# Kernel tuning notes

Hardware: AMD Instinct MI355X
Metric: run time of the kernel (lower is better)

The kernel has to match this reference:

```python
import jax, jax.numpy as jnp
import numpy as np

B, T = 2, 1000
IN_DIM, OUT_DIM = 257, 514
D_MODEL, D_STATE, D_CONV, EXPAND = 512, 16, 4, 2
D_INNER = EXPAND * D_MODEL          # 1024
DT_RANK = (D_MODEL + 15) // 16      # ceil(512/16) = 32
N_LAYER = 4
K_DC = 31                            # depthwise conv kernel in MambaDCLayer


def layer_norm(x, g, b, eps=1e-5):
    mu = jnp.mean(x, axis=-1, keepdims=True)
    var = jnp.mean((x - mu) ** 2, axis=-1, keepdims=True)
    return (x - mu) * jax.lax.rsqrt(var + eps) * g + b


def dw_conv1d(x, w, b, pad):
    # x: (B, T, C), w: (C, K) depthwise, pad: (left, right)
    y = jax.lax.conv_general_dilated(
        x.transpose(0, 2, 1), w[:, None, :], (1,), [pad],
        dimension_numbers=('NCH', 'OIH', 'NCH'), feature_group_count=w.shape[0])
    return (y + b[None, :, None]).transpose(0, 2, 1)


def mamba_block(x, W_in, conv_w, conv_b, W_x, W_dt, b_dt, A_log, Dp, W_out):
    # x: (B, T, d_model)
    xz = x @ W_in                               # (B, T, 2*D_INNER)
    xin, z = jnp.split(xz, 2, axis=-1)
    xin = dw_conv1d(xin, conv_w, conv_b, (D_CONV - 1, 0))  # causal depthwise conv
    xin = jax.nn.silu(xin)                      # (B, T, D_INNER)
    proj = xin @ W_x                            # (B, T, DT_RANK + 2*D_STATE)
    dt = jax.nn.softplus(proj[..., :DT_RANK] @ W_dt + b_dt)  # (B, T, D_INNER)
    Bm = proj[..., DT_RANK:DT_RANK + D_STATE]   # (B, T, D_STATE)
    Cm = proj[..., DT_RANK + D_STATE:]          # (B, T, D_STATE)
    A = -jnp.exp(A_log)                         # (D_INNER, D_STATE)
    dA = jnp.exp(dt[..., None] * A)             # (B, T, D_INNER, D_STATE)
    dBu = (dt * xin)[..., None] * Bm[:, :, None, :]  # (B, T, D_INNER, D_STATE)

    def step(h, inp):
        dA_t, dBu_t, C_t = inp
        h = dA_t * h + dBu_t
        return h, jnp.einsum('bds,bs->bd', h, C_t)

    h0 = jnp.zeros((x.shape[0], D_INNER, D_STATE), x.dtype)
    _, ys = jax.lax.scan(step, h0, (dA.transpose(1, 0, 2, 3),
                                    dBu.transpose(1, 0, 2, 3),
                                    Cm.transpose(1, 0, 2)))
    y = ys.transpose(1, 0, 2) + xin * Dp        # (B, T, D_INNER)
    y = y * jax.nn.silu(z)
    return y @ W_out                            # (B, T, d_model)


def setup_inputs() -> dict:
    key = jax.random.key(0)
    ks = iter(jax.random.split(key, 32))
    n = lambda shape, s=0.02: jax.random.normal(next(ks), shape, jnp.float32) * s
    return {
        'x': jax.random.normal(next(ks), (B, T, IN_DIM), jnp.float32),
        'lengths': jnp.full((B,), T, jnp.int32),
        'w_in0': n((IN_DIM, D_MODEL)),
        'ln_in_g': jnp.ones((D_MODEL,), jnp.float32),
        'ln_in_b': jnp.zeros((D_MODEL,), jnp.float32),
        'ln1_g': jnp.ones((N_LAYER, D_MODEL), jnp.float32),
        'ln1_b': jnp.zeros((N_LAYER, D_MODEL), jnp.float32),
        'W_inproj': n((N_LAYER, D_MODEL, 2 * D_INNER)),
        'conv_w': n((N_LAYER, D_INNER, D_CONV), 0.1),
        'conv_b': jnp.zeros((N_LAYER, D_INNER), jnp.float32),
        'W_xproj': n((N_LAYER, D_INNER, DT_RANK + 2 * D_STATE)),
        'W_dt': n((N_LAYER, DT_RANK, D_INNER), 0.1),
        'b_dt': jnp.full((N_LAYER, D_INNER), -4.6, jnp.float32),
        'A_log': jnp.tile(jnp.log(jnp.arange(1, D_STATE + 1, dtype=jnp.float32)),
                          (N_LAYER, D_INNER, 1)),
        'D': jnp.ones((N_LAYER, D_INNER), jnp.float32),
        'W_mo': n((N_LAYER, D_INNER, D_MODEL)),
        'ln2_g': jnp.ones((N_LAYER, D_MODEL), jnp.float32),
        'ln2_b': jnp.zeros((N_LAYER, D_MODEL), jnp.float32),
        'dc_w': n((N_LAYER, D_MODEL, K_DC), 0.1),
        'dc_b': jnp.zeros((N_LAYER, D_MODEL), jnp.float32),
        'w_out': n((D_MODEL, OUT_DIM)),
        'b_out': jnp.zeros((OUT_DIM,), jnp.float32),
    }


def reference(x, lengths, w_in0, ln_in_g, ln_in_b, ln1_g, ln1_b, W_inproj,
              conv_w, conv_b, W_xproj, W_dt, b_dt, A_log, D, W_mo,
              ln2_g, ln2_b, dc_w, dc_b, w_out, b_out):
    seq_mask = jnp.arange(x.shape[1]) < lengths[:, None]  # (B, T) bool
    h = jax.nn.relu(layer_norm(x @ w_in0, ln_in_g, ln_in_b))
    for i in range(N_LAYER):
        a = h + mamba_block(layer_norm(h, ln1_g[i], ln1_b[i]),
                            W_inproj[i], conv_w[i], conv_b[i], W_xproj[i],
                            W_dt[i], b_dt[i], A_log[i], D[i], W_mo[i])
        c = dw_conv1d(layer_norm(a, ln2_g[i], ln2_b[i]), dc_w[i], dc_b[i],
                      (K_DC // 2, K_DC // 2))  # 'same' padding
        h = a + c
    out = h @ w_out + b_out  # MagcIRM -> linear output head
    # lengths == T so output[seq_mask] is a full flatten to (B*T, OUT_DIM)
    out_flat = out.reshape(-1, out.shape[-1])
    return out_flat, seq_mask
```

## Files before the change

### kernel.cpp

```cpp
#include <hip/hip_runtime.h>
#include <cstdint>
#include <cstddef>

#define DEVI static __device__ __forceinline__

typedef unsigned short ushort_t;
typedef __attribute__((ext_vector_type(8))) short short8;
typedef __attribute__((ext_vector_type(4))) float f32x4;

DEVI float sp_softplus(float x) { return x > 20.f ? x : log1pf(__expf(x)); }
DEVI float silu_f(float x)      { return x / (1.f + __expf(-x)); }

DEVI ushort_t f2b(float v) {
    uint32_t u = __builtin_bit_cast(uint32_t, v);
    u += 0x7FFFu + ((u >> 16) & 1u);
    return (ushort_t)(u >> 16);
}
DEVI float b2f(ushort_t u) {
    uint32_t x = ((uint32_t)u) << 16;
    return __builtin_bit_cast(float, x);
}

DEVI void gload16(const ushort_t* g, ushort_t* l) {
    __builtin_amdgcn_global_load_lds(
        (const __attribute__((address_space(1))) unsigned int*)g,
        (__attribute__((address_space(3))) unsigned int*)l, 16, 0, 0);
}

#define NC 40
#define CL 25

template<bool RELU, bool OUTB16>
__global__ __launch_bounds__(256) void ln_k(const float* __restrict__ x,
                                            const float* __restrict__ g,
                                            const float* __restrict__ b,
                                            void* __restrict__ yv, int M)
{
    int wid  = threadIdx.x >> 6;
    int lane = threadIdx.x & 63;
    int row  = blockIdx.x * 4 + wid;
    if (row >= M) return;
    const float* xr = x + (size_t)row * 512;
    float4 v0 = *(const float4*)(xr + lane * 8);
    float4 v1 = *(const float4*)(xr + lane * 8 + 4);
    float vals[8] = {v0.x, v0.y, v0.z, v0.w, v1.x, v1.y, v1.z, v1.w};
    float s = 0.f;
#pragma unroll
    for (int i = 0; i < 8; i++) s += vals[i];
#pragma unroll
    for (int off = 1; off < 64; off <<= 1) s += __shfl_xor(s, off);
    float mu = s * (1.f / 512.f);
    float q = 0.f;
#pragma unroll
    for (int i = 0; i < 8; i++) { float d = vals[i] - mu; q += d * d; }
#pragma unroll
    for (int off = 1; off < 64; off <<= 1) q += __shfl_xor(q, off);
    float rstd = rsqrtf(q * (1.f / 512.f) + 1e-5f);
#pragma unroll
    for (int i = 0; i < 8; i++) {
        int c = lane * 8 + i;
        float o = (vals[i] - mu) * rstd * g[c] + b[c];
        if (RELU) o = fmaxf(o, 0.f);
        if (OUTB16) ((ushort_t*)yv)[(size_t)row * 512 + c] = f2b(o);
        else        ((float*)yv)[(size_t)row * 512 + c] = o;
    }
}

__global__ __launch_bounds__(256) void cvt_x_k(const float* __restrict__ x,
                                               ushort_t* __restrict__ xb)
{
    int e = blockIdx.x * 256 + threadIdx.x;
    if (e >= 2000 * 320) return;
    int k = e % 320, row = e / 320;
    xb[e] = (k < 257) ? f2b(x[(size_t)row * 257 + k]) : (ushort_t)0;
}

__global__ __launch_bounds__(256) void prep_small_k(const float* __restrict__ conv_w,
                                                    const float* __restrict__ dc_w,
                                                    const float* __restrict__ W_xproj,
                                                    float* __restrict__ cwt,
                                                    float* __restrict__ dcwt,
                                                    ushort_t* __restrict__ wxb)
{
    int e = blockIdx.x * 256 + threadIdx.x;
    if (e < 16384) {
        int l = e >> 12, rem = e & 4095, k = rem >> 10, d = rem & 1023;
        cwt[e] = conv_w[l * 4096 + d * 4 + k];
        return;
    }
    e -= 16384;
    if (e < 63488) {
        int l = e / 15872, rem = e % 15872, k = rem / 512, m = rem % 512;
        dcwt[e] = dc_w[l * 15872 + m * 31 + k];
        return;
    }
    e -= 63488;
    if (e < 262144) wxb[e] = f2b(W_xproj[e]);
}

__global__ __launch_bounds__(256) void tr_w_k(const float* __restrict__ src,
                                              ushort_t* __restrict__ dst,
                                              int Ktrue, int N, int ldo, int srcld,
                                              size_t sstride, size_t dstride)
{
    __shared__ float tile[32][33];
    src += blockIdx.z * sstride;
    dst += blockIdx.z * dstride;
    int n0 = blockIdx.x * 32, k0 = blockIdx.y * 32;
    int tx = threadIdx.x & 31, ty = threadIdx.x >> 5;
#pragma unroll
    for (int r = 0; r < 4; r++) {
        int k = k0 + ty + r * 8, n = n0 + tx;
        tile[ty + r * 8][tx] = (k < Ktrue && n < N) ? src[(size_t)k * srcld + n] : 0.f;
    }
    __syncthreads();
#pragma unroll
    for (int r = 0; r < 4; r++) {
        int n = n0 + ty + r * 8;
        if (n < N) dst[(size_t)n * ldo + k0 + tx] = f2b(tile[tx][ty + r * 8]);
    }
}

template<bool BIAS, int ACT, bool RES, bool OUTF32, bool OUTB16>
__global__ __launch_bounds__(256) void gemm6(
    const ushort_t* __restrict__ A, int lda,
    const ushort_t* __restrict__ Bt, int ldb,
    const float* __restrict__ bias,
    const float* __restrict__ R, int ldr,
    float* __restrict__ C, int ldc,
    ushort_t* __restrict__ C2, int ldc2,
    int M, int N, int K,
    size_t aStr, size_t bStr, size_t cStr)
{
    __shared__ ushort_t As[3][64 * 64];
    __shared__ ushort_t Bs[3][64 * 64];
    A  += blockIdx.z * aStr;
    Bt += blockIdx.z * bStr;
    C  += blockIdx.z * cStr;
    C2 += blockIdx.z * cStr;

    int tid = threadIdx.x;
    int wid = tid >> 6, l = tid & 63;
    int wr = wid >> 1, wc = wid & 1;
    int lk = l >> 4, lr = l & 15;
    int rhalf = tid >> 3, oct = tid & 7;

    int nwg = gridDim.x * gridDim.y;
    int bid = blockIdx.y * gridDim.x + blockIdx.x;
    {
        int q = nwg >> 3, r = nwg & 7;
        int xcd = bid & 7, lo = bid >> 3;
        bid = (xcd < r ? xcd * (q + 1) : r * (q + 1) + (xcd - r) * q) + lo;
    }
    int bx = bid % gridDim.x, by = bid / gridDim.x;
    int bm = by * 64, bn = bx * 64;

    f32x4 acc[2][2];
#pragma unroll
    for (int m = 0; m < 2; m++)
#pragma unroll
        for (int n = 0; n < 2; n++) acc[m][n] = (f32x4){0.f, 0.f, 0.f, 0.f};

    auto stage = [&](int buf, int k0) {
#pragma unroll
        for (int p = 0; p < 2; p++) {
            int row = p * 32 + rhalf;
            int cg = oct ^ (row & 7);
            gload16(A + (size_t)(bm + row) * lda + k0 + cg * 8,
                    &As[buf][p * 2048 + tid * 8]);
        }
#pragma unroll
        for (int p = 0; p < 2; p++) {
            int row = p * 32 + rhalf;
            int cg = oct ^ (row & 7);
            gload16(Bt + (size_t)(bn + row) * ldb + k0 + cg * 8,
                    &Bs[buf][p * 2048 + tid * 8]);
        }
    };

    auto compute = [&](int buf) {
#pragma unroll
        for (int kk = 0; kk < 2; kk++) {
            short8 af[2], bf[2];
#pragma unroll
            for (int m = 0; m < 2; m++) {
                int row = wr * 32 + m * 16 + lr;
                int sl = (kk * 4 + lk) ^ (row & 7);
                af[m] = *(const short8*)&As[buf][row * 64 + sl * 8];
            }
#pragma unroll
            for (int n = 0; n < 2; n++) {
                int col = wc * 32 + n * 16 + lr;
                int sl = (kk * 4 + lk) ^ (col & 7);
                bf[n] = *(const short8*)&Bs[buf][col * 64 + sl * 8];
            }
#pragma unroll
            for (int m = 0; m < 2; m++)
#pragma unroll
                for (int n = 0; n < 2; n++)
                    acc[m][n] = __builtin_amdgcn_mfma_f32_16x16x32_bf16(
                        af[m], bf[n], acc[m][n], 0, 0, 0);
        }
    };

    int nt = K >> 6;
    stage(0, 0);
    if (nt > 1) stage(1, 64);
    for (int t = 0; t < nt; t++) {
        if (t + 1 < nt) asm volatile("s_waitcnt vmcnt(4)" ::: "memory");
        else            asm volatile("s_waitcnt vmcnt(0)" ::: "memory");
        __builtin_amdgcn_s_barrier();
        if (t + 2 < nt) stage((t + 2) % 3, (t + 2) * 64);
        compute(t % 3);
    }

#pragma unroll
    for (int m = 0; m < 2; m++) {
#pragma unroll
        for (int n = 0; n < 2; n++) {
            int gn = bn + wc * 32 + n * 16 + lr;
            if (gn >= N) continue;
#pragma unroll
            for (int r = 0; r < 4; r++) {
                int gm = bm + wr * 32 + m * 16 + lk * 4 + r;
                if (gm >= M) continue;
                float v = acc[m][n][r];
                if (ACT == 2) {
                    if (gn < 1024) C2[(size_t)gm * ldc2 + gn] = f2b(sp_softplus(v + bias[gn]));
                    else ((float*)R)[(size_t)gm * ldr + (gn - 1024) + 32] = v;
                    continue;
                }
                if (BIAS) v += bias[gn];
                if (ACT == 1) v = sp_softplus(v);
                if (RES) v += R[(size_t)gm * ldr + gn];
                if (OUTF32) C[(size_t)gm * ldc + gn] = v;
                if (OUTB16) C2[(size_t)gm * ldc2 + gn] = f2b(v);
            }
        }
    }
}

__global__ __launch_bounds__(256) void conv4_silu_k(const ushort_t* __restrict__ xzb,
                                                    const float* __restrict__ cwt,
                                                    const float* __restrict__ bias,
                                                    ushort_t* __restrict__ xinb)
{
    int e = blockIdx.x * 256 + threadIdx.x;
    if (e >= 2000 * 128) return;
    int dg = (e & 127) * 8;
    int row = e >> 7;
    int b = row >= 1000 ? 1 : 0;
    int t = row - b * 1000;
    float acc[8];
#pragma unroll
    for (int j = 0; j < 8; j++) acc[j] = bias[dg + j];
#pragma unroll
    for (int k = 0; k < 4; k++) {
        int tt = t - 3 + k;
        if (tt < 0) continue;
        short8 v = *(const short8*)&xzb[(size_t)(b * 1000 + tt) * 2048 + dg];
#pragma unroll
        for (int j = 0; j < 8; j++)
            acc[j] += b2f((ushort_t)v[j]) * cwt[k * 1024 + dg + j];
    }
    short8 o;
#pragma unroll
    for (int j = 0; j < 8; j++) o[j] = (short)f2b(silu_f(acc[j]));
    *(short8*)&xinb[(size_t)row * 1024 + dg] = o;
}

__global__ __launch_bounds__(256) void scan_part1(const ushort_t* __restrict__ dt,
                                                  const ushort_t* __restrict__ xin,
                                                  const float* __restrict__ proj,
                                                  const float* __restrict__ A_log,
                                                  float* __restrict__ hloc,
                                                  float* __restrict__ sc)
{
    __shared__ ushort_t s_dt[CL][64], s_x[CL][64];
    __shared__ float s_B[CL][16];
    int d0 = blockIdx.x * 64;
    int c  = blockIdx.y;
    int b  = blockIdx.z;
    int tid = threadIdx.x;
    int ch = tid >> 2, st4 = tid & 3;
    int d = d0 + ch;
    int base = b * 1000 + c * CL;
    for (int lin = tid; lin < CL * 8; lin += 256) {
        int r = lin >> 3, q = lin & 7;
        size_t row = (size_t)(base + r);
        *(short8*)&s_dt[r][q * 8] = *(const short8*)&dt[row * 1024 + d0 + q * 8];
        *(short8*)&s_x[r][q * 8]  = *(const short8*)&xin[row * 1024 + d0 + q * 8];
    }
    for (int lin = tid; lin < CL * 16; lin += 256) {
        int r = lin >> 4, j = lin & 15;
        s_B[r][j] = proj[(size_t)(base + r) * 64 + 32 + j];
    }
    float4 alog = *(const float4*)&A_log[d * 16 + st4 * 4];
    float a_s[4] = {-__expf(alog.x), -__expf(alog.y), -__expf(alog.z), -__expf(alog.w)};
    __syncthreads();
    float h[4] = {0.f, 0.f, 0.f, 0.f};
    float sdt = 0.f;
#pragma unroll 5
    for (int t = 0; t < CL; t++) {
        float dtv = b2f(s_dt[t][ch]);
        float xv  = b2f(s_x[t][ch]);
        float4 Bv = *(const float4*)&s_B[t][st4 * 4];
        float dx = dtv * xv;
        sdt += dtv;
        h[0] = __expf(dtv * a_s[0]) * h[0] + dx * Bv.x;
        h[1] = __expf(dtv * a_s[1]) * h[1] + dx * Bv.y;
        h[2] = __expf(dtv * a_s[2]) * h[2] + dx * Bv.z;
        h[3] = __expf(dtv * a_s[3]) * h[3] + dx * Bv.w;
    }
    *(float4*)&hloc[((size_t)(b * NC + c) << 14) + ((size_t)d << 4) + st4 * 4] =
        (float4){h[0], h[1], h[2], h[3]};
    if (st4 == 0) sc[(b * NC + c) * 1024 + d] = sdt;
}

__global__ __launch_bounds__(256) void scan_combine(const float* __restrict__ A_log,
                                                    float* __restrict__ hloc,
                                                    const float* __restrict__ sc)
{
    int e = blockIdx.x * 256 + threadIdx.x;
    if (e >= 2 * 16384) return;
    int b = e >> 14;
    int rem = e & 16383;
    int dd = rem >> 4;
    float a_s = -__expf(A_log[rem]);
    float H = hloc[((size_t)(b * NC) << 14) + rem];
    for (int c = 1; c < NC; c++) {
        size_t idx = ((size_t)(b * NC + c) << 14) + rem;
        H = hloc[idx] + __expf(a_s * sc[(b * NC + c) * 1024 + dd]) * H;
        hloc[idx] = H;
    }
}

__global__ __launch_bounds__(256) void scan_part2(const ushort_t* __restrict__ dt,
                                                  const ushort_t* __restrict__ xin,
                                                  const float* __restrict__ proj,
                                                  const float* __restrict__ A_log,
                                                  const float* __restrict__ hend,
                                                  const float* __restrict__ Dp,
                                                  const ushort_t* __restrict__ xzb,
                                                  ushort_t* __restrict__ ysb)
{
    __shared__ ushort_t s_dt[CL][64], s_x[CL][64], s_y[CL][64];
    __shared__ float s_B[CL][16], s_C[CL][16];
    __shared__ float s_Dp[64];
    int d0 = blockIdx.x * 64;
    int c  = blockIdx.y;
    int b  = blockIdx.z;
    int tid = threadIdx.x;
    int ch = tid >> 2, st4 = tid & 3;
    int d = d0 + ch;
    int base = b * 1000 + c * CL;
    if (tid < 64) s_Dp[tid] = Dp[d0 + tid];
    for (int lin = tid; lin < CL * 8; lin += 256) {
        int r = lin >> 3, q = lin & 7;
        size_t row = (size_t)(base + r);
        *(short8*)&s_dt[r][q * 8] = *(const short8*)&dt[row * 1024 + d0 + q * 8];
        *(short8*)&s_x[r][q * 8]  = *(const short8*)&xin[row * 1024 + d0 + q * 8];
    }
    for (int lin = tid; lin < CL * 16; lin += 256) {
        int r = lin >> 4, j = lin & 15;
        s_B[r][j] = proj[(size_t)(base + r) * 64 + 32 + j];
        s_C[r][j] = proj[(size_t)(base + r) * 64 + 48 + j];
    }
    float4 alog = *(const float4*)&A_log[d * 16 + st4 * 4];
    float a_s[4] = {-__expf(alog.x), -__expf(alog.y), -__expf(alog.z), -__expf(alog.w)};
    float h[4] = {0.f, 0.f, 0.f, 0.f};
    if (c > 0) {
        float4 hv = *(const float4*)&hend[((size_t)(b * NC + c - 1) << 14)
                                          + ((size_t)d << 4) + st4 * 4];
        h[0] = hv.x; h[1] = hv.y; h[2] = hv.z; h[3] = hv.w;
    }
    __syncthreads();
#pragma unroll 5
    for (int t = 0; t < CL; t++) {
        float dtv = b2f(s_dt[t][ch]);
        float xv  = b2f(s_x[t][ch]);
        float4 Bv = *(const float4*)&s_B[t][st4 * 4];
        float4 Cv = *(const float4*)&s_C[t][st4 * 4];
        float dx = dtv * xv;
        h[0] = __expf(dtv * a_s[0]) * h[0] + dx * Bv.x;
        h[1] = __expf(dtv * a_s[1]) * h[1] + dx * Bv.y;
        h[2] = __expf(dtv * a_s[2]) * h[2] + dx * Bv.z;
        h[3] = __expf(dtv * a_s[3]) * h[3] + dx * Bv.w;
        float p = h[0] * Cv.x + h[1] * Cv.y + h[2] * Cv.z + h[3] * Cv.w;
        p += __shfl_xor(p, 1);
        p += __shfl_xor(p, 2);
        if (st4 == 0) s_y[t][ch] = f2b(p);
    }
    __syncthreads();
    for (int lin = tid; lin < CL * 8; lin += 256) {
        int r = lin >> 3, q = lin & 7;
        size_t row = (size_t)(base + r);
        int dd = d0 + q * 8;
        short8 yv = *(const short8*)&s_y[r][q * 8];
        short8 xv = *(const short8*)&s_x[r][q * 8];
        short8 zv = *(const short8*)&xzb[row * 2048 + 1024 + dd];
        short8 ov;
#pragma unroll
        for (int j = 0; j < 8; j++) {
            float o = (b2f((ushort_t)yv[j]) + b2f((ushort_t)xv[j]) * s_Dp[q * 8 + j])
                      * silu_f(b2f((ushort_t)zv[j]));
            ov[j] = (short)f2b(o);
        }
        *(short8*)&ysb[row * 1024 + dd] = ov;
    }
}

__global__ __launch_bounds__(256) void dcconv31_k(const float* __restrict__ ln,
                                                  const float* __restrict__ a,
                                                  const float* __restrict__ dcwt,
                                                  const float* __restrict__ bias,
                                                  float* __restrict__ h,
                                                  ushort_t* __restrict__ hb)
{
    int e = blockIdx.x * 256 + threadIdx.x;
    if (e >= 2000 * 512) return;
    int m = e & 511;
    int row = e >> 9;
    int b = row >= 1000 ? 1 : 0;
    int t = row - b * 1000;
    float acc = bias[m];
#pragma unroll
    for (int k = 0; k < 31; k++) {
        int tt = t - 15 + k;
        if (tt >= 0 && tt < 1000)
            acc += ln[((size_t)(b * 1000 + tt)) * 512 + m] * dcwt[k * 512 + m];
    }
    float v = a[e] + acc;
    h[e] = v;
    hb[e] = f2b(v);
}

__global__ void mask_k(const int* __restrict__ lengths, float* __restrict__ out)
{
    int i = blockIdx.x * 256 + threadIdx.x;
    if (i >= 2000) return;
    out[i] = ((i % 1000) < lengths[i / 1000]) ? 1.f : 0.f;
}

extern "C" void kernel_launch(void* const* d_in, const int* in_sizes, int n_in,
                              void* d_out, int out_size, void* d_ws, size_t ws_size,
                              hipStream_t stream)
{
    const float* x       = (const float*)d_in[0];
    const int*   lengths = (const int*)  d_in[1];
    const float* w_in0   = (const float*)d_in[2];
    const float* ln_in_g = (const float*)d_in[3];
    const float* ln_in_b = (const float*)d_in[4];
    const float* ln1_g   = (const float*)d_in[5];
    const float* ln1_b   = (const float*)d_in[6];
    const float* W_inproj= (const float*)d_in[7];
    const float* conv_w  = (const float*)d_in[8];
    const float* conv_b  = (const float*)d_in[9];
    const float* W_xproj = (const float*)d_in[10];
    const float* W_dt    = (const float*)d_in[11];
    const float* b_dt    = (const float*)d_in[12];
    const float* A_log   = (const float*)d_in[13];
    const float* Dp      = (const float*)d_in[14];
    const float* W_mo    = (const float*)d_in[15];
    const float* ln2_g   = (const float*)d_in[16];
    const float* ln2_b   = (const float*)d_in[17];
    const float* dc_w    = (const float*)d_in[18];
    const float* dc_b    = (const float*)d_in[19];
    const float* w_out   = (const float*)d_in[20];
    const float* b_out   = (const float*)d_in[21];

    char* p = (char*)d_ws;
    auto alloc_f = [&](size_t n) { float* r = (float*)p; p += n * 4; return r; };
    auto alloc_b = [&](size_t n) { ushort_t* r = (ushort_t*)p; p += n * 2; return r; };

    float* h    = alloc_f(2048 * 512);
    float* lnb  = alloc_f(2048 * 512);
    float* proj = alloc_f(2048 * 64);
    float* av   = alloc_f(2048 * 512);
    float* hloc = alloc_f((size_t)2 * NC * 16384);
    float* sc   = alloc_f((size_t)2 * NC * 1024);
    float* cwt  = alloc_f(4 * 4 * 1024);
    float* dcwt = alloc_f(4 * 31 * 512);
    ushort_t* xbf   = alloc_b(2048 * 320);
    ushort_t* lnbb  = alloc_b(2048 * 512);
    ushort_t* xzb   = alloc_b(2048 * 2048);
    ushort_t* xinb  = alloc_b(2048 * 1024);
    ushort_t* dtbb  = alloc_b(2048 * 1024);
    ushort_t* ysb   = alloc_b(2048 * 1024);
    ushort_t* hb    = alloc_b(2048 * 512);
    ushort_t* wt_in0 = alloc_b(512 * 320);
    ushort_t* wt_in  = alloc_b((size_t)4 * 2048 * 512);
    ushort_t* wt_dt  = alloc_b((size_t)4 * 1024 * 64);
    ushort_t* wt_mo  = alloc_b((size_t)4 * 512 * 1024);
    ushort_t* wt_out = alloc_b(576 * 512);
    ushort_t* wxb    = alloc_b((size_t)4 * 1024 * 64);
    ushort_t* wt_big = alloc_b((size_t)4 * 1152 * 1024);

    dim3 blk(256);

    cvt_x_k<<<(2000 * 320 + 255) / 256, blk, 0, stream>>>(x, xbf);
    prep_small_k<<<(16384 + 63488 + 262144 + 255) / 256, blk, 0, stream>>>(
        conv_w, dc_w, W_xproj, cwt, dcwt, wxb);
    tr_w_k<<<dim3(16, 10, 1), blk, 0, stream>>>(w_in0, wt_in0, 257, 512, 320, 512, 0, 0);
    tr_w_k<<<dim3(64, 16, 4), blk, 0, stream>>>(W_inproj, wt_in, 512, 2048, 512, 2048,
                                                (size_t)512 * 2048, (size_t)2048 * 512);
    tr_w_k<<<dim3(32, 2, 4),  blk, 0, stream>>>(W_dt, wt_dt, 32, 1024, 64, 1024,
                                                (size_t)32 * 1024, (size_t)1024 * 64);
    tr_w_k<<<dim3(16, 32, 4), blk, 0, stream>>>(W_mo, wt_mo, 1024, 512, 1024, 512,
                                                (size_t)1024 * 512, (size_t)512 * 1024);
    tr_w_k<<<dim3(17, 16, 1), blk, 0, stream>>>(w_out, wt_out, 512, 514, 512, 514, 0, 0);
    tr_w_k<<<dim3(1, 32, 4),  blk, 0, stream>>>(W_xproj + 32, wt_big + (size_t)1024 * 1024,
                                                1024, 32, 1024, 64,
                                                (size_t)1024 * 64, (size_t)1152 * 1024);
    gemm6<false, 0, false, false, true><<<dim3(16, 16, 4), blk, 0, stream>>>(
        wt_dt, 64, wxb, 64, nullptr, nullptr, 0, nullptr, 0, wt_big, 1024,
        1024, 1024, 64,
        (size_t)1024 * 64, (size_t)1024 * 64, (size_t)1152 * 1024);

    gemm6<false, 0, false, true, false><<<dim3(8, 32), blk, 0, stream>>>(
        xbf, 320, wt_in0, 320, nullptr, nullptr, 0, lnb, 512, nullptr, 0,
        2000, 512, 320, 0, 0, 0);
    ln_k<true, false><<<500, blk, 0, stream>>>(lnb, ln_in_g, ln_in_b, h, 2000);

    for (int i = 0; i < 4; i++) {
        const float* Al = A_log + (size_t)i * 16384;
        ln_k<false, true><<<500, blk, 0, stream>>>(h, ln1_g + i * 512, ln1_b + i * 512,
                                                   lnbb, 2000);
        gemm6<false, 0, false, false, true><<<dim3(32, 32), blk, 0, stream>>>(
            lnbb, 512, wt_in + (size_t)i * 2048 * 512, 512,
            nullptr, nullptr, 0, nullptr, 0, xzb, 2048, 2000, 2048, 512, 0, 0, 0);
        conv4_silu_k<<<1000, blk, 0, stream>>>(xzb, cwt + i * 4096,
                                               conv_b + i * 1024, xinb);
        gemm6<false, 2, false, false, false><<<dim3(17, 32), blk, 0, stream>>>(
            xinb, 1024, wt_big + (size_t)i * 1152 * 1024, 1024,
            b_dt + i * 1024, proj, 64, nullptr, 0, dtbb, 1024, 2000, 1056, 1024, 0, 0, 0);
        scan_part1<<<dim3(16, NC, 2), blk, 0, stream>>>(dtbb, xinb, proj, Al, hloc, sc);
        scan_combine<<<128, blk, 0, stream>>>(Al, hloc, sc);
        scan_part2<<<dim3(16, NC, 2), blk, 0, stream>>>(dtbb, xinb, proj, Al, hloc,
                                                        Dp + i * 1024, xzb, ysb);
        gemm6<false, 0, true, true, false><<<dim3(8, 32), blk, 0, stream>>>(
            ysb, 1024, wt_mo + (size_t)i * 512 * 1024, 1024,
            nullptr, h, 512, av, 512, nullptr, 0, 2000, 512, 1024, 0, 0, 0);
        ln_k<false, false><<<500, blk, 0, stream>>>(av, ln2_g + i * 512, ln2_b + i * 512,
                                                    lnb, 2000);
        dcconv31_k<<<4000, blk, 0, stream>>>(lnb, av, dcwt + i * 31 * 512,
                                             dc_b + i * 512, h, hb);
    }

    gemm6<true, 0, false, true, false><<<dim3(9, 32), blk, 0, stream>>>(
        hb, 512, wt_out, 512, b_out, nullptr, 0, (float*)d_out, 514, nullptr, 0,
        2000, 514, 512, 0, 0, 0);
    mask_k<<<8, blk, 0, stream>>>(lengths, (float*)d_out + 2000 * 514);
}
```

Measured before the change: 516.7 us.

## Fuse chunked scan passes into one kernel with inter-block flag sync; bf16 LN2 output

Merges the three-kernel chunked selective scan (local pass, serial combine, second pass) into one kernel. Chunk-0 blocks spin until all chunks publish local states, then propagate the carried state and raise per-chunk flags that later-chunk blocks wait on. This removes two launches and reloading dt/x/B into shared memory, but depends on all blocks being co-resident to avoid deadlock, and the combine serialises through chunk-0 blocks with a syncthreads per chunk. Separately, the second layernorm now writes bf16 and the depthwise conv reads bf16, halving that traffic at some precision cost.

```diff
diff --git a/kernel.cpp b/kernel.cpp
--- a/kernel.cpp
+++ b/kernel.cpp
@@ -269,22 +269,27 @@
     *(short8*)&xinb[(size_t)row * 1024 + dg] = o;
 }
 
-__global__ __launch_bounds__(256) void scan_part1(const ushort_t* __restrict__ dt,
-                                                  const ushort_t* __restrict__ xin,
-                                                  const float* __restrict__ proj,
-                                                  const float* __restrict__ A_log,
-                                                  float* __restrict__ hloc,
-                                                  float* __restrict__ sc)
-{
-    __shared__ ushort_t s_dt[CL][64], s_x[CL][64];
-    __shared__ float s_B[CL][16];
-    int d0 = blockIdx.x * 64;
-    int c  = blockIdx.y;
-    int b  = blockIdx.z;
+__global__ __launch_bounds__(256, 5) void scan_fused(
+    const ushort_t* __restrict__ dt, const ushort_t* __restrict__ xin,
+    const float* __restrict__ proj, const float* __restrict__ A_log,
+    const float* __restrict__ Dp, const ushort_t* __restrict__ xzb,
+    ushort_t* __restrict__ ysb, float* __restrict__ hloc,
+    float* __restrict__ sc, unsigned* __restrict__ cnt,
+    unsigned* __restrict__ pflag)
+{
+    __shared__ ushort_t s_dt[CL][64], s_x[CL][64], s_y[CL][64];
+    __shared__ float s_B[CL][16], s_C[CL][16];
+    __shared__ float s_Dp[64];
+    int x = blockIdx.x, c = blockIdx.y, b = blockIdx.z;
+    int d0 = x * 64;
     int tid = threadIdx.x;
     int ch = tid >> 2, st4 = tid & 3;
     int d = d0 + ch;
     int base = b * 1000 + c * CL;
+    unsigned* mycnt = cnt + b * 16 + x;
+    unsigned* mypf  = pflag + (size_t)(b * 16 + x) * NC;
+
+    if (tid < 64) s_Dp[tid] = Dp[d0 + tid];
     for (int lin = tid; lin < CL * 8; lin += 256) {
         int r = lin >> 3, q = lin & 7;
         size_t row = (size_t)(base + r);
@@ -294,10 +299,12 @@
     for (int lin = tid; lin < CL * 16; lin += 256) {
         int r = lin >> 4, j = lin & 15;
         s_B[r][j] = proj[(size_t)(base + r) * 64 + 32 + j];
+        s_C[r][j] = proj[(size_t)(base + r) * 64 + 48 + j];
     }
     float4 alog = *(const float4*)&A_log[d * 16 + st4 * 4];
     float a_s[4] = {-__expf(alog.x), -__expf(alog.y), -__expf(alog.z), -__expf(alog.w)};
     __syncthreads();
+
     float h[4] = {0.f, 0.f, 0.f, 0.f};
     float sdt = 0.f;
 #pragma unroll 5
@@ -312,69 +319,56 @@
         h[2] = __expf(dtv * a_s[2]) * h[2] + dx * Bv.z;
         h[3] = __expf(dtv * a_s[3]) * h[3] + dx * Bv.w;
     }
-    *(float4*)&hloc[((size_t)(b * NC + c) << 14) + ((size_t)d << 4) + st4 * 4] =
-        (float4){h[0], h[1], h[2], h[3]};
+    size_t hidx = ((size_t)(b * NC + c) << 14) + ((size_t)d << 4) + st4 * 4;
+    *(float4*)&hloc[hidx] = (float4){h[0], h[1], h[2], h[3]};
     if (st4 == 0) sc[(b * NC + c) * 1024 + d] = sdt;
-}
-
-__global__ __launch_bounds__(256) void scan_combine(const float* __restrict__ A_log,
-                                                    float* __restrict__ hloc,
-                                                    const float* __restrict__ sc)
-{
-    int e = blockIdx.x * 256 + threadIdx.x;
-    if (e >= 2 * 16384) return;
-    int b = e >> 14;
-    int rem = e & 16383;
-    int dd = rem >> 4;
-    float a_s = -__expf(A_log[rem]);
-    float H = hloc[((size_t)(b * NC) << 14) + rem];
-    for (int c = 1; c < NC; c++) {
-        size_t idx = ((size_t)(b * NC + c) << 14) + rem;
-        H = hloc[idx] + __expf(a_s * sc[(b * NC + c) * 1024 + dd]) * H;
-        hloc[idx] = H;
-    }
-}
-
-__global__ __launch_bounds__(256) void scan_part2(const ushort_t* __restrict__ dt,
-                                                  const ushort_t* __restrict__ xin,
-                                                  const float* __restrict__ proj,
-                                                  const float* __restrict__ A_log,
-                                                  const float* __restrict__ hend,
-                                                  const float* __restrict__ Dp,
-                                                  const ushort_t* __restrict__ xzb,
-                                                  ushort_t* __restrict__ ysb)
-{
-    __shared__ ushort_t s_dt[CL][64], s_x[CL][64], s_y[CL][64];
-    __shared__ float s_B[CL][16], s_C[CL][16];
-    __shared__ float s_Dp[64];
-    int d0 = blockIdx.x * 64;
-    int c  = blockIdx.y;
-    int b  = blockIdx.z;
-    int tid = threadIdx.x;
-    int ch = tid >> 2, st4 = tid & 3;
-    int d = d0 + ch;
-    int base = b * 1000 + c * CL;
-    if (tid < 64) s_Dp[tid] = Dp[d0 + tid];
-    for (int lin = tid; lin < CL * 8; lin += 256) {
-        int r = lin >> 3, q = lin & 7;
-        size_t row = (size_t)(base + r);
-        *(short8*)&s_dt[r][q * 8] = *(const short8*)&dt[row * 1024 + d0 + q * 8];
-        *(short8*)&s_x[r][q * 8]  = *(const short8*)&xin[row * 1024 + d0 + q * 8];
-    }
-    for (int lin = tid; lin < CL * 16; lin += 256) {
-        int r = lin >> 4, j = lin & 15;
-        s_B[r][j] = proj[(size_t)(base + r) * 64 + 32 + j];
-        s_C[r][j] = proj[(size_t)(base + r) * 64 + 48 + j];
-    }
-    float4 alog = *(const float4*)&A_log[d * 16 + st4 * 4];
-    float a_s[4] = {-__expf(alog.x), -__expf(alog.y), -__expf(alog.z), -__expf(alog.w)};
-    float h[4] = {0.f, 0.f, 0.f, 0.f};
-    if (c > 0) {
-        float4 hv = *(const float4*)&hend[((size_t)(b * NC + c - 1) << 14)
+    __threadfence();
+    __syncthreads();
+    if (tid == 0) {
+        atomicAdd(mycnt, 1u);
+        if (c == 0) atomicExch(&mypf[0], 1u);
+    }
+
+    float hs[4] = {0.f, 0.f, 0.f, 0.f};
+    if (c == 0) {
+        while (atomicAdd(mycnt, 0u) < NC) __builtin_amdgcn_s_sleep(2);
+        __threadfence();
+        float H[4] = {h[0], h[1], h[2], h[3]};
+        for (int cb = 1; cb < NC; cb += 8) {
+            float4 hv[8]; float sv[8];
+#pragma unroll
+            for (int j = 0; j < 8; j++) {
+                if (cb + j < NC) {
+                    hv[j] = *(const float4*)&hloc[((size_t)(b * NC + cb + j) << 14)
+                                                  + ((size_t)d << 4) + st4 * 4];
+                    sv[j] = sc[(b * NC + cb + j) * 1024 + d];
+                }
+            }
+#pragma unroll
+            for (int j = 0; j < 8; j++) {
+                if (cb + j < NC) {
+                    H[0] = hv[j].x + __expf(a_s[0] * sv[j]) * H[0];
+                    H[1] = hv[j].y + __expf(a_s[1] * sv[j]) * H[1];
+                    H[2] = hv[j].z + __expf(a_s[2] * sv[j]) * H[2];
+                    H[3] = hv[j].w + __expf(a_s[3] * sv[j]) * H[3];
+                    *(float4*)&hloc[((size_t)(b * NC + cb + j) << 14)
+                                    + ((size_t)d << 4) + st4 * 4] =
+                        (float4){H[0], H[1], H[2], H[3]};
+                    __threadfence();
+                    __syncthreads();
+                    if (tid == 0) atomicExch(&mypf[cb + j], 1u);
+                }
+            }
+        }
+    } else {
+        while (atomicAdd(&mypf[c - 1], 0u) == 0u) __builtin_amdgcn_s_sleep(2);
+        __threadfence();
+        float4 hv = *(const float4*)&hloc[((size_t)(b * NC + c - 1) << 14)
                                           + ((size_t)d << 4) + st4 * 4];
-        h[0] = hv.x; h[1] = hv.y; h[2] = hv.z; h[3] = hv.w;
-    }
-    __syncthreads();
+        hs[0] = hv.x; hs[1] = hv.y; hs[2] = hv.z; hs[3] = hv.w;
+    }
+
+    h[0] = hs[0]; h[1] = hs[1]; h[2] = hs[2]; h[3] = hs[3];
 #pragma unroll 5
     for (int t = 0; t < CL; t++) {
         float dtv = b2f(s_dt[t][ch]);
@@ -410,7 +404,7 @@
     }
 }
 
-__global__ __launch_bounds__(256) void dcconv31_k(const float* __restrict__ ln,
+__global__ __launch_bounds__(256) void dcconv31_k(const ushort_t* __restrict__ ln,
                                                   const float* __restrict__ a,
                                                   const float* __restrict__ dcwt,
                                                   const float* __restrict__ bias,
@@ -428,7 +422,7 @@
     for (int k = 0; k < 31; k++) {
         int tt = t - 15 + k;
         if (tt >= 0 && tt < 1000)
-            acc += ln[((size_t)(b * 1000 + tt)) * 512 + m] * dcwt[k * 512 + m];
+            acc += b2f(ln[((size_t)(b * 1000 + tt)) * 512 + m]) * dcwt[k * 512 + m];
     }
     float v = a[e] + acc;
     h[e] = v;
@@ -472,6 +466,7 @@
     char* p = (char*)d_ws;
     auto alloc_f = [&](size_t n) { float* r = (float*)p; p += n * 4; return r; };
     auto alloc_b = [&](size_t n) { ushort_t* r = (ushort_t*)p; p += n * 2; return r; };
+    auto alloc_u = [&](size_t n) { unsigned* r = (unsigned*)p; p += n * 4; return r; };
 
     float* h    = alloc_f(2048 * 512);
     float* lnb  = alloc_f(2048 * 512);
@@ -481,6 +476,7 @@
     float* sc   = alloc_f((size_t)2 * NC * 1024);
     float* cwt  = alloc_f(4 * 4 * 1024);
     float* dcwt = alloc_f(4 * 31 * 512);
+    unsigned* flags = alloc_u(4 * (32 + 32 * NC));
     ushort_t* xbf   = alloc_b(2048 * 320);
     ushort_t* lnbb  = alloc_b(2048 * 512);
     ushort_t* xzb   = alloc_b(2048 * 2048);
@@ -497,6 +493,8 @@
     ushort_t* wt_big = alloc_b((size_t)4 * 1152 * 1024);
 
     dim3 blk(256);
+
+    hipMemsetAsync(flags, 0, (size_t)4 * (32 + 32 * NC) * 4, stream);
 
     cvt_x_k<<<(2000 * 320 + 255) / 256, blk, 0, stream>>>(x, xbf);
     prep_small_k<<<(16384 + 63488 + 262144 + 255) / 256, blk, 0, stream>>>(
@@ -524,6 +522,8 @@
 
     for (int i = 0; i < 4; i++) {
         const float* Al = A_log + (size_t)i * 16384;
+        unsigned* cnt_i = flags + (size_t)i * (32 + 32 * NC);
+        unsigned* pf_i  = cnt_i + 32;
         ln_k<false, true><<<500, blk, 0, stream>>>(h, ln1_g + i * 512, ln1_b + i * 512,
                                                    lnbb, 2000);
         gemm6<false, 0, false, false, true><<<dim3(32, 32), blk, 0, stream>>>(
@@ -534,16 +534,14 @@
         gemm6<false, 2, false, false, false><<<dim3(17, 32), blk, 0, stream>>>(
             xinb, 1024, wt_big + (size_t)i * 1152 * 1024, 1024,
             b_dt + i * 1024, proj, 64, nullptr, 0, dtbb, 1024, 2000, 1056, 1024, 0, 0, 0);
-        scan_part1<<<dim3(16, NC, 2), blk, 0, stream>>>(dtbb, xinb, proj, Al, hloc, sc);
-        scan_combine<<<128, blk, 0, stream>>>(Al, hloc, sc);
-        scan_part2<<<dim3(16, NC, 2), blk, 0, stream>>>(dtbb, xinb, proj, Al, hloc,
-                                                        Dp + i * 1024, xzb, ysb);
+        scan_fused<<<dim3(16, NC, 2), blk, 0, stream>>>(
+            dtbb, xinb, proj, Al, Dp + i * 1024, xzb, ysb, hloc, sc, cnt_i, pf_i);
         gemm6<false, 0, true, true, false><<<dim3(8, 32), blk, 0, stream>>>(
             ysb, 1024, wt_mo + (size_t)i * 512 * 1024, 1024,
             nullptr, h, 512, av, 512, nullptr, 0, 2000, 512, 1024, 0, 0, 0);
-        ln_k<false, false><<<500, blk, 0, stream>>>(av, ln2_g + i * 512, ln2_b + i * 512,
-                                                    lnb, 2000);
-        dcconv31_k<<<4000, blk, 0, stream>>>(lnb, av, dcwt + i * 31 * 512,
+        ln_k<false, true><<<500, blk, 0, stream>>>(av, ln2_g + i * 512, ln2_b + i * 512,
+                                                   lnbb, 2000);
+        dcconv31_k<<<4000, blk, 0, stream>>>(lnbb, av, dcwt + i * 31 * 512,
                                              dc_b + i * 512, h, hb);
     }
 
```

Result: slower. 1.783 ms (+245.0%).

## Unfold precomposed W_x·W_dt into two-stage x_proj then dt_proj GEMMs

Applied to the files above, without the earlier changes.

Drops the setup-time precomposition of W_xproj and W_dt into a 1152-wide weight. Instead each layer runs a small 64-column x_proj GEMM, which writes proj in fp32 plus a bf16 copy of the dt-rank slice, then a K=64 dt GEMM with bias and softplus. This cuts the FLOPs of the per-layer wide GEMM and removes the setup GEMM, at the cost of an extra launch and a very low-parallelism 64-column GEMM. Separately, the second LayerNorm now writes bf16 and the 31-tap conv reads bf16, halving that traffic at some precision cost.

```diff
diff --git a/kernel.cpp b/kernel.cpp
--- a/kernel.cpp
+++ b/kernel.cpp
@@ -77,10 +77,8 @@
 
 __global__ __launch_bounds__(256) void prep_small_k(const float* __restrict__ conv_w,
                                                     const float* __restrict__ dc_w,
-                                                    const float* __restrict__ W_xproj,
                                                     float* __restrict__ cwt,
-                                                    float* __restrict__ dcwt,
-                                                    ushort_t* __restrict__ wxb)
+                                                    float* __restrict__ dcwt)
 {
     int e = blockIdx.x * 256 + threadIdx.x;
     if (e < 16384) {
@@ -92,10 +90,7 @@
     if (e < 63488) {
         int l = e / 15872, rem = e % 15872, k = rem / 512, m = rem % 512;
         dcwt[e] = dc_w[l * 15872 + m * 31 + k];
-        return;
-    }
-    e -= 63488;
-    if (e < 262144) wxb[e] = f2b(W_xproj[e]);
+    }
 }
 
 __global__ __launch_bounds__(256) void tr_w_k(const float* __restrict__ src,
@@ -225,9 +220,10 @@
                 int gm = bm + wr * 32 + m * 16 + lk * 4 + r;
                 if (gm >= M) continue;
                 float v = acc[m][n][r];
-                if (ACT == 2) {
-                    if (gn < 1024) C2[(size_t)gm * ldc2 + gn] = f2b(sp_softplus(v + bias[gn]));
-                    else ((float*)R)[(size_t)gm * ldr + (gn - 1024) + 32] = v;
+                if (ACT == 3) {
+                    if (gn < 32) C2[(size_t)gm * ldc2 + gn] = f2b(v);
+                    else { C[(size_t)gm * ldc + gn] = v;
+                           C2[(size_t)gm * ldc2 + gn] = 0; }
                     continue;
                 }
                 if (BIAS) v += bias[gn];
@@ -410,7 +406,7 @@
     }
 }
 
-__global__ __launch_bounds__(256) void dcconv31_k(const float* __restrict__ ln,
+__global__ __launch_bounds__(256) void dcconv31_k(const ushort_t* __restrict__ ln,
                                                   const float* __restrict__ a,
                                                   const float* __restrict__ dcwt,
                                                   const float* __restrict__ bias,
@@ -428,7 +424,7 @@
     for (int k = 0; k < 31; k++) {
         int tt = t - 15 + k;
         if (tt >= 0 && tt < 1000)
-            acc += ln[((size_t)(b * 1000 + tt)) * 512 + m] * dcwt[k * 512 + m];
+            acc += b2f(ln[((size_t)(b * 1000 + tt)) * 512 + m]) * dcwt[k * 512 + m];
     }
     float v = a[e] + acc;
     h[e] = v;
@@ -488,19 +484,19 @@
     ushort_t* dtbb  = alloc_b(2048 * 1024);
     ushort_t* ysb   = alloc_b(2048 * 1024);
     ushort_t* hb    = alloc_b(2048 * 512);
+    ushort_t* projb = alloc_b(2048 * 64);
     ushort_t* wt_in0 = alloc_b(512 * 320);
     ushort_t* wt_in  = alloc_b((size_t)4 * 2048 * 512);
     ushort_t* wt_dt  = alloc_b((size_t)4 * 1024 * 64);
     ushort_t* wt_mo  = alloc_b((size_t)4 * 512 * 1024);
     ushort_t* wt_out = alloc_b(576 * 512);
-    ushort_t* wxb    = alloc_b((size_t)4 * 1024 * 64);
-    ushort_t* wt_big = alloc_b((size_t)4 * 1152 * 1024);
+    ushort_t* wxt    = alloc_b((size_t)4 * 64 * 1024);
 
     dim3 blk(256);
 
     cvt_x_k<<<(2000 * 320 + 255) / 256, blk, 0, stream>>>(x, xbf);
-    prep_small_k<<<(16384 + 63488 + 262144 + 255) / 256, blk, 0, stream>>>(
-        conv_w, dc_w, W_xproj, cwt, dcwt, wxb);
+    prep_small_k<<<(16384 + 63488 + 255) / 256, blk, 0, stream>>>(
+        conv_w, dc_w, cwt, dcwt);
     tr_w_k<<<dim3(16, 10, 1), blk, 0, stream>>>(w_in0, wt_in0, 257, 512, 320, 512, 0, 0);
     tr_w_k<<<dim3(64, 16, 4), blk, 0, stream>>>(W_inproj, wt_in, 512, 2048, 512, 2048,
                                                 (size_t)512 * 2048, (size_t)2048 * 512);
@@ -509,13 +505,8 @@
     tr_w_k<<<dim3(16, 32, 4), blk, 0, stream>>>(W_mo, wt_mo, 1024, 512, 1024, 512,
                                                 (size_t)1024 * 512, (size_t)512 * 1024);
     tr_w_k<<<dim3(17, 16, 1), blk, 0, stream>>>(w_out, wt_out, 512, 514, 512, 514, 0, 0);
-    tr_w_k<<<dim3(1, 32, 4),  blk, 0, stream>>>(W_xproj + 32, wt_big + (size_t)1024 * 1024,
-                                                1024, 32, 1024, 64,
-                                                (size_t)1024 * 64, (size_t)1152 * 1024);
-    gemm6<false, 0, false, false, true><<<dim3(16, 16, 4), blk, 0, stream>>>(
-        wt_dt, 64, wxb, 64, nullptr, nullptr, 0, nullptr, 0, wt_big, 1024,
-        1024, 1024, 64,
-        (size_t)1024 * 64, (size_t)1024 * 64, (size_t)1152 * 1024);
+    tr_w_k<<<dim3(2, 32, 4),  blk, 0, stream>>>(W_xproj, wxt, 1024, 64, 1024, 64,
+                                                (size_t)1024 * 64, (size_t)64 * 1024);
 
     gemm6<false, 0, false, true, false><<<dim3(8, 32), blk, 0, stream>>>(
         xbf, 320, wt_in0, 320, nullptr, nullptr, 0, lnb, 512, nullptr, 0,
@@ -531,9 +522,13 @@
             nullptr, nullptr, 0, nullptr, 0, xzb, 2048, 2000, 2048, 512, 0, 0, 0);
         conv4_silu_k<<<1000, blk, 0, stream>>>(xzb, cwt + i * 4096,
                                                conv_b + i * 1024, xinb);
-        gemm6<false, 2, false, false, false><<<dim3(17, 32), blk, 0, stream>>>(
-            xinb, 1024, wt_big + (size_t)i * 1152 * 1024, 1024,
-            b_dt + i * 1024, proj, 64, nullptr, 0, dtbb, 1024, 2000, 1056, 1024, 0, 0, 0);
+        gemm6<false, 3, false, false, false><<<dim3(1, 32), blk, 0, stream>>>(
+            xinb, 1024, wxt + (size_t)i * 64 * 1024, 1024,
+            nullptr, nullptr, 0, proj, 64, projb, 64, 2000, 64, 1024, 0, 0, 0);
+        gemm6<true, 1, false, false, true><<<dim3(16, 32), blk, 0, stream>>>(
+            projb, 64, wt_dt + (size_t)i * 1024 * 64, 64,
+            b_dt + i * 1024, nullptr, 0, nullptr, 0, dtbb, 1024,
+            2000, 1024, 64, 0, 0, 0);
         scan_part1<<<dim3(16, NC, 2), blk, 0, stream>>>(dtbb, xinb, proj, Al, hloc, sc);
         scan_combine<<<128, blk, 0, stream>>>(Al, hloc, sc);
         scan_part2<<<dim3(16, NC, 2), blk, 0, stream>>>(dtbb, xinb, proj, Al, hloc,
@@ -541,9 +536,9 @@
         gemm6<false, 0, true, true, false><<<dim3(8, 32), blk, 0, stream>>>(
             ysb, 1024, wt_mo + (size_t)i * 512 * 1024, 1024,
             nullptr, h, 512, av, 512, nullptr, 0, 2000, 512, 1024, 0, 0, 0);
-        ln_k<false, false><<<500, blk, 0, stream>>>(av, ln2_g + i * 512, ln2_b + i * 512,
-                                                    lnb, 2000);
-        dcconv31_k<<<4000, blk, 0, stream>>>(lnb, av, dcwt + i * 31 * 512,
+        ln_k<false, true><<<500, blk, 0, stream>>>(av, ln2_g + i * 512, ln2_b + i * 512,
+                                                   lnbb, 2000);
+        dcconv31_k<<<4000, blk, 0, stream>>>(lnbb, av, dcwt + i * 31 * 512,
                                              dc_b + i * 512, h, hb);
     }
 
```

Result: slower. 527.8 us (+2.1%).
